# Performance work log

Measured on AMD Instinct MI355X. Metric: run time of the kernel, lower is better.

Reference implementation:

```python
import jax, jax.numpy as jnp
import numpy as np

N_NODES = 100000
N_EDGES = 1600000
D_NODE = 128
D_EDGE = 64
HID = 128
HEADS = 4
N_LAYERS = 3
LN_EPS = 1e-5
NEG_SLOPE = 0.2


def setup_inputs() -> dict:
    key = jax.random.key(0)
    ks = jax.random.split(key, 16)
    s = 0.05
    inp = {
        "node_features": jax.random.normal(ks[0], (N_NODES, D_NODE), jnp.float32),
        "edge_index": jax.random.randint(ks[1], (2, N_EDGES), 0, N_NODES, jnp.int32),
        "edge_attr": jax.random.normal(ks[2], (N_EDGES, D_EDGE), jnp.float32),
        # node encoder
        "W0": jax.random.normal(ks[3], (D_NODE, HID), jnp.float32) * s,
        "b0": jnp.zeros((HID,), jnp.float32),
        # per-layer stacked params [L, ...]
        "We": jax.random.normal(ks[4], (N_LAYERS, D_EDGE, HID), jnp.float32) * s,  # edge_encoder weight
        "be": jnp.zeros((N_LAYERS, HID), jnp.float32),
        "Wg": jax.random.normal(ks[5], (N_LAYERS, HID, HEADS * HID), jnp.float32) * s,  # GAT lin
        "att_src": jax.random.normal(ks[6], (N_LAYERS, HEADS, HID), jnp.float32) * s,
        "att_dst": jax.random.normal(ks[7], (N_LAYERS, HEADS, HID), jnp.float32) * s,
        "bg": jnp.zeros((N_LAYERS, HID), jnp.float32),  # GAT bias
        "gamma": jnp.ones((N_LAYERS, HID), jnp.float32),  # LayerNorm
        "beta": jnp.zeros((N_LAYERS, HID), jnp.float32),
    }
    return inp


def _layer_norm(x, g, b):
    mu = x.mean(-1, keepdims=True)
    var = ((x - mu) ** 2).mean(-1, keepdims=True)
    return (x - mu) * jax.lax.rsqrt(var + LN_EPS) * g + b


def _gat(x, src, dst, ew, Wg, att_s, att_d, bias, n):
    # x: [N,HID]; GATConv(heads=4, concat=False): average heads, +bias
    h = (x @ Wg).reshape(n, HEADS, HID)                     # [N,H,C]
    a_s = jnp.einsum("nhc,hc->nh", h, att_s)                # [N,H]
    a_d = jnp.einsum("nhc,hc->nh", h, att_d)
    logits = jax.nn.leaky_relu(a_s[src] + a_d[dst] + ew[:, None], NEG_SLOPE)  # [E,H]
    # segment softmax over incoming edges of each dst node
    m = jax.ops.segment_max(logits, dst, num_segments=n)    # self-loops => every node covered
    ex = jnp.exp(logits - m[dst])
    denom = jax.ops.segment_sum(ex, dst, num_segments=n)
    alpha = ex / denom[dst]                                 # [E,H]
    outs = []
    for hd in range(HEADS):  # loop over fixed small head count to cap peak memory
        msg = alpha[:, hd:hd + 1] * h[src, hd, :]           # [E,C]
        outs.append(jax.ops.segment_sum(msg, dst, num_segments=n))
    return jnp.stack(outs, 1).mean(1) + bias                # [N,HID]


def reference(node_features, edge_index, edge_attr, W0, b0, We, be, Wg, att_src, att_dst, bg, gamma, beta):
    n = node_features.shape[0]
    src, dst = edge_index[0], edge_index[1]
    # add self-loops (PyG GATConv default)
    loop = jnp.arange(n, dtype=src.dtype)
    src_f = jnp.concatenate([src, loop])
    dst_f = jnp.concatenate([dst, loop])

    x = jax.nn.relu(node_features @ W0 + b0)                # dropout = identity in eval
    for l in range(N_LAYERS):
        # edge_encoder(edge_attr).mean(-1) -> scalar edge weight added to attention logits
        ew = (edge_attr @ We[l] + be[l]).mean(-1)           # [E]
        ew_f = jnp.concatenate([ew, jnp.full((n,), ew.mean(), ew.dtype)])  # 'mean' fill for self-loops
        y = _gat(x, src_f, dst_f, ew_f, Wg[l], att_src[l], att_dst[l], bg[l], n)
        y = _layer_norm(y, gamma[l], beta[l])
        x = jax.nn.relu(x + y)
    return x
```

## Files before the change

### kernel.cpp

```cpp
#include <hip/hip_runtime.h>
#include <hip/hip_bf16.h>
#include <cstdio>

#define N_NODES 100000
#define N_EDGES 1600000
#define D_NODE 128
#define D_EDGE 64
#define HID 128
#define HEADS 4
#define N_LAYERS 3
#define LN_EPS 1e-5f
#define NEG_SLOPE 0.2f
#define EE (N_EDGES + N_NODES)
#define EW_GRID ((N_EDGES + 255) / 256)
#define SCAN_THREADS 1024
#define SCAN_CHUNK ((N_NODES + SCAN_THREADS - 1) / SCAN_THREADS)

typedef unsigned short bfraw;
using bf16x8 = __attribute__((ext_vector_type(8))) short;
using f32x4  = __attribute__((ext_vector_type(4))) float;

__device__ __forceinline__ float b2f(bfraw u) {
    return __uint_as_float(((unsigned)u) << 16);
}
__device__ __forceinline__ bfraw f2b(float f) {
    unsigned u = __float_as_uint(f);
    unsigned r = (u + 0x7fffu + ((u >> 16) & 1u)) >> 16;
    return (bfraw)r;
}
__device__ __forceinline__ float lrelu(float v) {
    return v > 0.f ? v : NEG_SLOPE * v;
}

__global__ __launch_bounds__(256) void prep_kernel(
    const float* __restrict__ We, const float* __restrict__ be,
    float* __restrict__ wem, float* __restrict__ bem) {
    int tid = threadIdx.x;
    if (tid < N_LAYERS * D_EDGE) {
        int l = tid / D_EDGE, d = tid % D_EDGE;
        const float* row = We + ((size_t)l * D_EDGE + d) * HID;
        float s = 0.f;
        for (int j = 0; j < HID; j++) s += row[j];
        wem[tid] = s * (1.0f / HID);
    } else if (tid < N_LAYERS * D_EDGE + N_LAYERS) {
        int l = tid - N_LAYERS * D_EDGE;
        const float* row = be + (size_t)l * HID;
        float s = 0.f;
        for (int j = 0; j < HID; j++) s += row[j];
        bem[l] = s * (1.0f / HID);
    }
}

__global__ __launch_bounds__(256) void ew_kernel(
    const float* __restrict__ ea, const float* __restrict__ wem,
    const float* __restrict__ bem, float* __restrict__ ew,
    float* __restrict__ partial) {
    __shared__ float wsh[N_LAYERS * D_EDGE];
    __shared__ float bsh[N_LAYERS];
    __shared__ float red[4][3];
    int tid = threadIdx.x;
    if (tid < N_LAYERS * D_EDGE) wsh[tid] = wem[tid];
    if (tid < N_LAYERS) bsh[tid] = bem[tid];
    __syncthreads();
    long long e = (long long)blockIdx.x * 256 + tid;
    float d0 = 0.f, d1 = 0.f, d2 = 0.f;
    if (e < N_EDGES) {
        const float4* row = (const float4*)(ea + (size_t)e * D_EDGE);
#pragma unroll
        for (int i = 0; i < D_EDGE / 4; i++) {
            float4 v = row[i];
            int c = i * 4;
            d0 += v.x * wsh[c] + v.y * wsh[c + 1] + v.z * wsh[c + 2] + v.w * wsh[c + 3];
            d1 += v.x * wsh[64 + c] + v.y * wsh[64 + c + 1] + v.z * wsh[64 + c + 2] + v.w * wsh[64 + c + 3];
            d2 += v.x * wsh[128 + c] + v.y * wsh[128 + c + 1] + v.z * wsh[128 + c + 2] + v.w * wsh[128 + c + 3];
        }
        ew[e] = d0 + bsh[0];
        ew[(size_t)N_EDGES + e] = d1 + bsh[1];
        ew[2 * (size_t)N_EDGES + e] = d2 + bsh[2];
    }
    float s0 = d0, s1 = d1, s2 = d2;
    for (int o = 32; o; o >>= 1) {
        s0 += __shfl_xor(s0, o);
        s1 += __shfl_xor(s1, o);
        s2 += __shfl_xor(s2, o);
    }
    int wid = tid >> 6;
    if ((tid & 63) == 0) {
        red[wid][0] = s0;
        red[wid][1] = s1;
        red[wid][2] = s2;
    }
    __syncthreads();
    if (tid < 3) {
        partial[(size_t)tid * EW_GRID + blockIdx.x] =
            red[0][tid] + red[1][tid] + red[2][tid] + red[3][tid];
    }
}

__global__ __launch_bounds__(256) void ewred_kernel(
    const float* __restrict__ partial, const float* __restrict__ bem,
    float* __restrict__ ewsum) {
    __shared__ float red[4];
    int l = blockIdx.x;
    int tid = threadIdx.x;
    float s = 0.f;
    for (int i = tid; i < EW_GRID; i += 256) s += partial[(size_t)l * EW_GRID + i];
    for (int o = 32; o; o >>= 1) s += __shfl_xor(s, o);
    int wid = tid >> 6;
    if ((tid & 63) == 0) red[wid] = s;
    __syncthreads();
    if (tid == 0)
        ewsum[l] = red[0] + red[1] + red[2] + red[3] + bem[l] * (float)N_EDGES;
}

__global__ __launch_bounds__(256) void deginit_kernel(int* __restrict__ deg) {
    int i = blockIdx.x * 256 + threadIdx.x;
    if (i < N_NODES) deg[i] = 1;
}

__global__ __launch_bounds__(256) void hist_kernel(
    const int* __restrict__ ei, int* __restrict__ deg) {
    int e = blockIdx.x * 256 + threadIdx.x;
    if (e < N_EDGES) atomicAdd(&deg[ei[N_EDGES + e]], 1);
}

__global__ __launch_bounds__(SCAN_THREADS) void scan_kernel(
    const int* __restrict__ deg, int* __restrict__ rowptr, int* __restrict__ woff) {
    __shared__ int part[SCAN_THREADS];
    int tid = threadIdx.x;
    int lo = tid * SCAN_CHUNK;
    int hi = lo + SCAN_CHUNK < N_NODES ? lo + SCAN_CHUNK : N_NODES;
    int s = 0;
    for (int i = lo; i < hi; i++) s += deg[i];
    part[tid] = s;
    __syncthreads();
    for (int off = 1; off < SCAN_THREADS; off <<= 1) {
        int t = (tid >= off) ? part[tid - off] : 0;
        __syncthreads();
        part[tid] += t;
        __syncthreads();
    }
    int run = (tid == 0) ? 0 : part[tid - 1];
    for (int i = lo; i < hi; i++) {
        rowptr[i] = run;
        woff[i] = run + 1;
        run += deg[i];
    }
    if (tid == 0) rowptr[N_NODES] = EE;
}

__global__ __launch_bounds__(256) void scatter_kernel(
    const int* __restrict__ ei, const float* __restrict__ ew,
    int* __restrict__ woff, int* __restrict__ csr_src,
    float* __restrict__ csr_ew) {
    int e = blockIdx.x * 256 + threadIdx.x;
    if (e >= N_EDGES) return;
    int d = ei[N_EDGES + e];
    int pos = atomicAdd(&woff[d], 1);
    csr_src[pos] = ei[e];
    csr_ew[pos] = ew[e];
    csr_ew[(size_t)EE + pos] = ew[(size_t)N_EDGES + e];
    csr_ew[2 * (size_t)EE + pos] = ew[2 * (size_t)N_EDGES + e];
}

__global__ __launch_bounds__(256) void selfloop_kernel(
    const int* __restrict__ rowptr, const float* __restrict__ ewsum,
    int* __restrict__ csr_src, float* __restrict__ csr_ew) {
    int d = blockIdx.x * 256 + threadIdx.x;
    if (d >= N_NODES) return;
    int pos = rowptr[d];
    csr_src[pos] = d;
    csr_ew[pos] = ewsum[0] * (1.0f / N_EDGES);
    csr_ew[(size_t)EE + pos] = ewsum[1] * (1.0f / N_EDGES);
    csr_ew[2 * (size_t)EE + pos] = ewsum[2] * (1.0f / N_EDGES);
}

__global__ __launch_bounds__(256) void castnf_kernel(
    const float* __restrict__ in, bfraw* __restrict__ out, int n4) {
    int i = blockIdx.x * 256 + threadIdx.x;
    if (i >= n4) return;
    float4 v = *(const float4*)(in + (size_t)i * 4);
    ushort4 u;
    u.x = f2b(v.x); u.y = f2b(v.y); u.z = f2b(v.z); u.w = f2b(v.w);
    *(ushort4*)(out + (size_t)i * 4) = u;
}

__global__ __launch_bounds__(256) void tcast_kernel(
    const float* __restrict__ in, bfraw* __restrict__ out, int lgN, int total) {
    int t = blockIdx.x * 256 + threadIdx.x;
    if (t >= total) return;
    int k = t & 127;
    int n = (t >> 7) & ((1 << lgN) - 1);
    int l = t >> (7 + lgN);
    out[t] = f2b(in[((size_t)l << (7 + lgN)) + ((size_t)k << lgN) + n]);
}

template <int EPI>
__global__ __launch_bounds__(256) void gemm_mfma_kernel(
    const bfraw* __restrict__ A, const bfraw* __restrict__ Bt,
    const float* __restrict__ bias, bfraw* __restrict__ outb,
    float* __restrict__ outf, int M, int N) {
    __shared__ short Alds[64 * 136];
    __shared__ short Blds[64 * 136];
    int tid = threadIdx.x;
    int m0 = blockIdx.y * 64;
    int n0 = blockIdx.x * 64;
    {
        int li = tid;
#pragma unroll
        for (int i = 0; i < 4; i++, li += 256) {
            int row = li >> 4, ch = li & 15;
            uint4 v = make_uint4(0u, 0u, 0u, 0u);
            if (m0 + row < M)
                v = *(const uint4*)(A + (size_t)(m0 + row) * 128 + ch * 8);
            *(uint4*)&Alds[row * 136 + ch * 8] = v;
            uint4 bv = *(const uint4*)(Bt + (size_t)(n0 + row) * 128 + ch * 8);
            *(uint4*)&Blds[row * 136 + ch * 8] = bv;
        }
    }
    __syncthreads();
    int w = tid >> 6, lane = tid & 63;
    int quad = lane >> 4, lr = lane & 15;
    bf16x8 bfr[4];
#pragma unroll
    for (int kc = 0; kc < 4; kc++)
        bfr[kc] = *(const bf16x8*)&Blds[(w * 16 + lr) * 136 + kc * 32 + quad * 8];
#pragma unroll
    for (int mt = 0; mt < 4; mt++) {
        f32x4 acc = {0.f, 0.f, 0.f, 0.f};
#pragma unroll
        for (int kc = 0; kc < 4; kc++) {
            bf16x8 afr = *(const bf16x8*)&Alds[(mt * 16 + lr) * 136 + kc * 32 + quad * 8];
            acc = __builtin_amdgcn_mfma_f32_16x16x32_bf16(afr, bfr[kc], acc, 0, 0, 0);
        }
        int col = n0 + w * 16 + lr;
#pragma unroll
        for (int r = 0; r < 4; r++) {
            int row = m0 + mt * 16 + quad * 4 + r;
            if (row >= M) continue;
            float v = acc[r];
            if (EPI == 1) {
                v += bias[col];
                v = fmaxf(v, 0.f);
                outf[(size_t)row * 128 + col] = v;
                outb[(size_t)row * 128 + col] = f2b(v);
            } else {
                outb[(size_t)row * N + col] = f2b(v);
            }
        }
    }
}

__global__ __launch_bounds__(256) void att_kernel(
    const bfraw* __restrict__ h, const float* __restrict__ att_s_l,
    const float* __restrict__ att_d_l, float* __restrict__ a_s, float* __restrict__ a_d) {
    __shared__ float ss[HEADS * HID], sd[HEADS * HID];
    int tid = threadIdx.x;
    for (int i = tid; i < HEADS * HID; i += 256) {
        ss[i] = att_s_l[i];
        sd[i] = att_d_l[i];
    }
    __syncthreads();
    long long gid = (long long)blockIdx.x * 256 + tid;
    if (gid >= (long long)N_NODES * HEADS) return;
    int n = (int)(gid >> 2), hd = (int)(gid & 3);
    const uint4* hv = (const uint4*)(h + (size_t)n * (HEADS * HID) + hd * HID);
    const float* ssp = ss + hd * HID;
    const float* sdp = sd + hd * HID;
    float s = 0.f, d = 0.f;
#pragma unroll
    for (int i = 0; i < 16; i++) {
        uint4 u = hv[i];
        unsigned wv[4] = {u.x, u.y, u.z, u.w};
#pragma unroll
        for (int j = 0; j < 4; j++) {
            float lo = __uint_as_float(wv[j] << 16);
            float hi = __uint_as_float(wv[j] & 0xffff0000u);
            int c = i * 8 + j * 2;
            s += lo * ssp[c] + hi * ssp[c + 1];
            d += lo * sdp[c] + hi * sdp[c + 1];
        }
    }
    a_s[gid] = s;
    a_d[gid] = d;
}

__device__ __forceinline__ void accum8(float* acc, uint4 u, float e) {
    unsigned wv[4] = {u.x, u.y, u.z, u.w};
#pragma unroll
    for (int j = 0; j < 4; j++) {
        acc[2 * j]     += e * __uint_as_float(wv[j] << 16);
        acc[2 * j + 1] += e * __uint_as_float(wv[j] & 0xffff0000u);
    }
}

__global__ __launch_bounds__(256) void agg_sm_ln_kernel(
    const int* __restrict__ rowptr, const int* __restrict__ csr_src,
    const float* __restrict__ ewl, const float* __restrict__ a_s,
    const float* __restrict__ a_d, const bfraw* __restrict__ h,
    const float* __restrict__ bg, const float* __restrict__ gamma,
    const float* __restrict__ beta, float* __restrict__ x, bfraw* __restrict__ xb) {
    int node = blockIdx.x * 4 + (threadIdx.x >> 6);
    int lane = threadIdx.x & 63;
    if (node >= N_NODES) return;
    int head = lane >> 4;
    int c8 = (lane & 15) * 8;
    int rs = rowptr[node], re = rowptr[node + 1];
    float ad = a_d[(size_t)node * HEADS + head];
    const bfraw* hb = h + head * HID + c8;

    float m = -1e30f, den = 0.f;
    float acc[8];
#pragma unroll
    for (int k = 0; k < 8; k++) acc[k] = 0.f;

    int i = rs;
    for (; i + 4 <= re; i += 4) {
        int s0 = csr_src[i],     s1 = csr_src[i + 1];
        int s2 = csr_src[i + 2], s3 = csr_src[i + 3];
        float w0 = ewl[i],     w1 = ewl[i + 1];
        float w2 = ewl[i + 2], w3 = ewl[i + 3];
        uint4 u0 = *(const uint4*)(hb + (size_t)s0 * (HEADS * HID));
        uint4 u1 = *(const uint4*)(hb + (size_t)s1 * (HEADS * HID));
        uint4 u2 = *(const uint4*)(hb + (size_t)s2 * (HEADS * HID));
        uint4 u3 = *(const uint4*)(hb + (size_t)s3 * (HEADS * HID));
        float as0 = a_s[(size_t)s0 * HEADS + head];
        float as1 = a_s[(size_t)s1 * HEADS + head];
        float as2 = a_s[(size_t)s2 * HEADS + head];
        float as3 = a_s[(size_t)s3 * HEADS + head];
        float l0 = lrelu(as0 + ad + w0);
        float l1 = lrelu(as1 + ad + w1);
        float l2 = lrelu(as2 + ad + w2);
        float l3 = lrelu(as3 + ad + w3);
        float mx = fmaxf(fmaxf(l0, l1), fmaxf(l2, l3));
        if (mx > m) {
            float c = __expf(m - mx);
            den *= c;
#pragma unroll
            for (int k = 0; k < 8; k++) acc[k] *= c;
            m = mx;
        }
        float e0 = __expf(l0 - m), e1 = __expf(l1 - m);
        float e2 = __expf(l2 - m), e3 = __expf(l3 - m);
        den += e0 + e1 + e2 + e3;
        accum8(acc, u0, e0);
        accum8(acc, u1, e1);
        accum8(acc, u2, e2);
        accum8(acc, u3, e3);
    }
    for (; i < re; i++) {
        int s = csr_src[i];
        float w = ewl[i];
        uint4 u = *(const uint4*)(hb + (size_t)s * (HEADS * HID));
        float as = a_s[(size_t)s * HEADS + head];
        float l0 = lrelu(as + ad + w);
        if (l0 > m) {
            float c = __expf(m - l0);
            den *= c;
#pragma unroll
            for (int k = 0; k < 8; k++) acc[k] *= c;
            m = l0;
        }
        float e = __expf(l0 - m);
        den += e;
        accum8(acc, u, e);
    }

    float iv = 1.f / den;
    float y[8];
    float sum = 0.f;
#pragma unroll
    for (int k = 0; k < 8; k++) {
        float v = acc[k] * iv;
        v += __shfl_xor(v, 16);
        v += __shfl_xor(v, 32);
        y[k] = 0.25f * v + bg[c8 + k];
        sum += y[k];
    }
#pragma unroll
    for (int o = 8; o; o >>= 1) sum += __shfl_xor(sum, o);
    float mu = sum * (1.f / HID);
    float vs = 0.f;
#pragma unroll
    for (int k = 0; k < 8; k++) {
        float d = y[k] - mu;
        vs += d * d;
    }
#pragma unroll
    for (int o = 8; o; o >>= 1) vs += __shfl_xor(vs, o);
    float r = rsqrtf(vs * (1.f / HID) + LN_EPS);

    if (lane < 16) {
        float4 xv0 = *(const float4*)(x + (size_t)node * HID + c8);
        float4 xv1 = *(const float4*)(x + (size_t)node * HID + c8 + 4);
        float xv[8] = {xv0.x, xv0.y, xv0.z, xv0.w, xv1.x, xv1.y, xv1.z, xv1.w};
        float o8[8];
#pragma unroll
        for (int k = 0; k < 8; k++) {
            float o = (y[k] - mu) * r * gamma[c8 + k] + beta[c8 + k];
            o8[k] = fmaxf(xv[k] + o, 0.f);
        }
        *(float4*)(x + (size_t)node * HID + c8) = make_float4(o8[0], o8[1], o8[2], o8[3]);
        *(float4*)(x + (size_t)node * HID + c8 + 4) = make_float4(o8[4], o8[5], o8[6], o8[7]);
        uint4 ub;
        ub.x = (unsigned)f2b(o8[0]) | ((unsigned)f2b(o8[1]) << 16);
        ub.y = (unsigned)f2b(o8[2]) | ((unsigned)f2b(o8[3]) << 16);
        ub.z = (unsigned)f2b(o8[4]) | ((unsigned)f2b(o8[5]) << 16);
        ub.w = (unsigned)f2b(o8[6]) | ((unsigned)f2b(o8[7]) << 16);
        *(uint4*)(xb + (size_t)node * HID + c8) = ub;
    }
}

extern "C" void kernel_launch(void* const* d_in, const int* in_sizes, int n_in,
                              void* d_out, int out_size, void* d_ws, size_t ws_size,
                              hipStream_t stream) {
    const float* nf      = (const float*)d_in[0];
    const int*   ei      = (const int*)d_in[1];
    const float* ea      = (const float*)d_in[2];
    const float* W0      = (const float*)d_in[3];
    const float* b0      = (const float*)d_in[4];
    const float* We      = (const float*)d_in[5];
    const float* be      = (const float*)d_in[6];
    const float* Wg      = (const float*)d_in[7];
    const float* att_src = (const float*)d_in[8];
    const float* att_dst = (const float*)d_in[9];
    const float* bg      = (const float*)d_in[10];
    const float* gamma   = (const float*)d_in[11];
    const float* beta    = (const float*)d_in[12];
    float* x = (float*)d_out;

    char* p = (char*)d_ws;
    auto alloc = [&](size_t bytes) -> void* {
        void* r = (void*)p;
        p += (bytes + 255) & ~(size_t)255;
        return r;
    };
    bfraw*  h       = (bfraw*)alloc((size_t)N_NODES * HEADS * HID * sizeof(bfraw));
    float4* alpha   = (float4*)alloc((size_t)EE * sizeof(float4));
    bfraw*  xb      = (bfraw*)alloc((size_t)N_NODES * HID * sizeof(bfraw));
    float*  a_s     = (float*)alloc((size_t)N_NODES * HEADS * sizeof(float));
    float*  a_d     = (float*)alloc((size_t)N_NODES * HEADS * sizeof(float));
    float*  ew      = (float*)alloc((size_t)N_LAYERS * N_EDGES * sizeof(float));
    int*    csr_src = (int*)alloc((size_t)EE * sizeof(int));
    float*  csr_ew  = (float*)alloc((size_t)N_LAYERS * EE * sizeof(float));
    int*    rowptr  = (int*)alloc((size_t)(N_NODES + 1) * sizeof(int));
    int*    deg     = (int*)alloc((size_t)N_NODES * sizeof(int));
    int*    woff    = (int*)alloc((size_t)N_NODES * sizeof(int));
    float*  wem     = (float*)alloc((size_t)N_LAYERS * D_EDGE * sizeof(float));
    float*  bem     = (float*)alloc((size_t)N_LAYERS * sizeof(float));
    float*  ewsum   = (float*)alloc((size_t)N_LAYERS * sizeof(float));
    float*  partial = (float*)alloc((size_t)N_LAYERS * EW_GRID * sizeof(float));
    bfraw*  W0bt    = (bfraw*)alloc((size_t)HID * D_NODE * sizeof(bfraw));
    bfraw*  Wgbt    = (bfraw*)alloc((size_t)N_LAYERS * HEADS * HID * HID * sizeof(bfraw));
    size_t need = (size_t)(p - (char*)d_ws);
    if (need > ws_size) {
        fprintf(stderr, "kernel_launch: workspace too small: need %zu have %zu\n", need, ws_size);
        return;
    }
    bfraw* nfb = (bfraw*)alpha;

    prep_kernel<<<1, 256, 0, stream>>>(We, be, wem, bem);
    ew_kernel<<<EW_GRID, 256, 0, stream>>>(ea, wem, bem, ew, partial);
    ewred_kernel<<<N_LAYERS, 256, 0, stream>>>(partial, bem, ewsum);

    deginit_kernel<<<(N_NODES + 255) / 256, 256, 0, stream>>>(deg);
    hist_kernel<<<(N_EDGES + 255) / 256, 256, 0, stream>>>(ei, deg);
    scan_kernel<<<1, SCAN_THREADS, 0, stream>>>(deg, rowptr, woff);
    scatter_kernel<<<(N_EDGES + 255) / 256, 256, 0, stream>>>(ei, ew, woff, csr_src, csr_ew);
    selfloop_kernel<<<(N_NODES + 255) / 256, 256, 0, stream>>>(rowptr, ewsum, csr_src, csr_ew);

    castnf_kernel<<<((N_NODES * D_NODE / 4) + 255) / 256, 256, 0, stream>>>(
        nf, nfb, N_NODES * D_NODE / 4);
    tcast_kernel<<<(HID * D_NODE + 255) / 256, 256, 0, stream>>>(
        W0, W0bt, 7, HID * D_NODE);
    tcast_kernel<<<(N_LAYERS * HID * HEADS * HID + 255) / 256, 256, 0, stream>>>(
        Wg, Wgbt, 9, N_LAYERS * HID * HEADS * HID);

    gemm_mfma_kernel<1><<<dim3(HID / 64, (N_NODES + 63) / 64), 256, 0, stream>>>(
        nfb, W0bt, b0, xb, x, N_NODES, HID);

    for (int l = 0; l < N_LAYERS; l++) {
        gemm_mfma_kernel<0><<<dim3(HEADS * HID / 64, (N_NODES + 63) / 64), 256, 0, stream>>>(
            xb, Wgbt + (size_t)l * HEADS * HID * HID, nullptr, h, nullptr,
            N_NODES, HEADS * HID);
        att_kernel<<<((long long)N_NODES * HEADS + 255) / 256, 256, 0, stream>>>(
            h, att_src + (size_t)l * HEADS * HID, att_dst + (size_t)l * HEADS * HID, a_s, a_d);
        agg_sm_ln_kernel<<<(N_NODES + 3) / 4, 256, 0, stream>>>(
            rowptr, csr_src, csr_ew + (size_t)l * EE, a_s, a_d, h,
            bg + (size_t)l * HID, gamma + (size_t)l * HID,
            beta + (size_t)l * HID, x, xb);
    }
}
```

Before: 2.126 ms.

## Pack CSR src and edge weights into uint4, fuse edge-weight with scatter

Fuses the edge-weight projection into the CSR scatter kernel, which now writes one packed uint4 record (src index plus three per-layer weights) per edge. This removes the intermediate ew buffer and the separate scatter pass. The aggregation kernel is templated on layer to select its weight field, unrolled to 8 edges per iteration, and uses a lazy max rescale threshold of 8 to skip most rescaling. The trade-offs are that each layer reads 16 bytes per edge instead of 8, and the lazy rescale lets exponent arguments grow up to about 8.

```diff
diff --git a/kernel.cpp b/kernel.cpp
--- a/kernel.cpp
+++ b/kernel.cpp
@@ -51,68 +51,6 @@
     }
 }
 
-__global__ __launch_bounds__(256) void ew_kernel(
-    const float* __restrict__ ea, const float* __restrict__ wem,
-    const float* __restrict__ bem, float* __restrict__ ew,
-    float* __restrict__ partial) {
-    __shared__ float wsh[N_LAYERS * D_EDGE];
-    __shared__ float bsh[N_LAYERS];
-    __shared__ float red[4][3];
-    int tid = threadIdx.x;
-    if (tid < N_LAYERS * D_EDGE) wsh[tid] = wem[tid];
-    if (tid < N_LAYERS) bsh[tid] = bem[tid];
-    __syncthreads();
-    long long e = (long long)blockIdx.x * 256 + tid;
-    float d0 = 0.f, d1 = 0.f, d2 = 0.f;
-    if (e < N_EDGES) {
-        const float4* row = (const float4*)(ea + (size_t)e * D_EDGE);
-#pragma unroll
-        for (int i = 0; i < D_EDGE / 4; i++) {
-            float4 v = row[i];
-            int c = i * 4;
-            d0 += v.x * wsh[c] + v.y * wsh[c + 1] + v.z * wsh[c + 2] + v.w * wsh[c + 3];
-            d1 += v.x * wsh[64 + c] + v.y * wsh[64 + c + 1] + v.z * wsh[64 + c + 2] + v.w * wsh[64 + c + 3];
-            d2 += v.x * wsh[128 + c] + v.y * wsh[128 + c + 1] + v.z * wsh[128 + c + 2] + v.w * wsh[128 + c + 3];
-        }
-        ew[e] = d0 + bsh[0];
-        ew[(size_t)N_EDGES + e] = d1 + bsh[1];
-        ew[2 * (size_t)N_EDGES + e] = d2 + bsh[2];
-    }
-    float s0 = d0, s1 = d1, s2 = d2;
-    for (int o = 32; o; o >>= 1) {
-        s0 += __shfl_xor(s0, o);
-        s1 += __shfl_xor(s1, o);
-        s2 += __shfl_xor(s2, o);
-    }
-    int wid = tid >> 6;
-    if ((tid & 63) == 0) {
-        red[wid][0] = s0;
-        red[wid][1] = s1;
-        red[wid][2] = s2;
-    }
-    __syncthreads();
-    if (tid < 3) {
-        partial[(size_t)tid * EW_GRID + blockIdx.x] =
-            red[0][tid] + red[1][tid] + red[2][tid] + red[3][tid];
-    }
-}
-
-__global__ __launch_bounds__(256) void ewred_kernel(
-    const float* __restrict__ partial, const float* __restrict__ bem,
-    float* __restrict__ ewsum) {
-    __shared__ float red[4];
-    int l = blockIdx.x;
-    int tid = threadIdx.x;
-    float s = 0.f;
-    for (int i = tid; i < EW_GRID; i += 256) s += partial[(size_t)l * EW_GRID + i];
-    for (int o = 32; o; o >>= 1) s += __shfl_xor(s, o);
-    int wid = tid >> 6;
-    if ((tid & 63) == 0) red[wid] = s;
-    __syncthreads();
-    if (tid == 0)
-        ewsum[l] = red[0] + red[1] + red[2] + red[3] + bem[l] * (float)N_EDGES;
-}
-
 __global__ __launch_bounds__(256) void deginit_kernel(int* __restrict__ deg) {
     int i = blockIdx.x * 256 + threadIdx.x;
     if (i < N_NODES) deg[i] = 1;
@@ -149,30 +87,87 @@
     if (tid == 0) rowptr[N_NODES] = EE;
 }
 
-__global__ __launch_bounds__(256) void scatter_kernel(
-    const int* __restrict__ ei, const float* __restrict__ ew,
-    int* __restrict__ woff, int* __restrict__ csr_src,
-    float* __restrict__ csr_ew) {
-    int e = blockIdx.x * 256 + threadIdx.x;
-    if (e >= N_EDGES) return;
-    int d = ei[N_EDGES + e];
-    int pos = atomicAdd(&woff[d], 1);
-    csr_src[pos] = ei[e];
-    csr_ew[pos] = ew[e];
-    csr_ew[(size_t)EE + pos] = ew[(size_t)N_EDGES + e];
-    csr_ew[2 * (size_t)EE + pos] = ew[2 * (size_t)N_EDGES + e];
+__global__ __launch_bounds__(256) void ewscat_kernel(
+    const float* __restrict__ ea, const int* __restrict__ ei,
+    const float* __restrict__ wem, const float* __restrict__ bem,
+    int* __restrict__ woff, uint4* __restrict__ csrq,
+    float* __restrict__ partial) {
+    __shared__ float wsh[N_LAYERS * D_EDGE];
+    __shared__ float bsh[N_LAYERS];
+    __shared__ float red[4][3];
+    int tid = threadIdx.x;
+    if (tid < N_LAYERS * D_EDGE) wsh[tid] = wem[tid];
+    if (tid < N_LAYERS) bsh[tid] = bem[tid];
+    __syncthreads();
+    long long e = (long long)blockIdx.x * 256 + tid;
+    float d0 = 0.f, d1 = 0.f, d2 = 0.f;
+    if (e < N_EDGES) {
+        const float4* row = (const float4*)(ea + (size_t)e * D_EDGE);
+#pragma unroll
+        for (int i = 0; i < D_EDGE / 4; i++) {
+            float4 v = row[i];
+            int c = i * 4;
+            d0 += v.x * wsh[c] + v.y * wsh[c + 1] + v.z * wsh[c + 2] + v.w * wsh[c + 3];
+            d1 += v.x * wsh[64 + c] + v.y * wsh[64 + c + 1] + v.z * wsh[64 + c + 2] + v.w * wsh[64 + c + 3];
+            d2 += v.x * wsh[128 + c] + v.y * wsh[128 + c + 1] + v.z * wsh[128 + c + 2] + v.w * wsh[128 + c + 3];
+        }
+        int src = ei[e];
+        int dst = ei[N_EDGES + e];
+        int pos = atomicAdd(&woff[dst], 1);
+        uint4 q;
+        q.x = (unsigned)src;
+        q.y = __float_as_uint(d0 + bsh[0]);
+        q.z = __float_as_uint(d1 + bsh[1]);
+        q.w = __float_as_uint(d2 + bsh[2]);
+        csrq[pos] = q;
+    }
+    float s0 = d0, s1 = d1, s2 = d2;
+    for (int o = 32; o; o >>= 1) {
+        s0 += __shfl_xor(s0, o);
+        s1 += __shfl_xor(s1, o);
+        s2 += __shfl_xor(s2, o);
+    }
+    int wid = tid >> 6;
+    if ((tid & 63) == 0) {
+        red[wid][0] = s0;
+        red[wid][1] = s1;
+        red[wid][2] = s2;
+    }
+    __syncthreads();
+    if (tid < 3) {
+        partial[(size_t)tid * EW_GRID + blockIdx.x] =
+            red[0][tid] + red[1][tid] + red[2][tid] + red[3][tid];
+    }
+}
+
+__global__ __launch_bounds__(256) void ewred_kernel(
+    const float* __restrict__ partial, const float* __restrict__ bem,
+    float* __restrict__ ewsum) {
+    __shared__ float red[4];
+    int l = blockIdx.x;
+    int tid = threadIdx.x;
+    float s = 0.f;
+    for (int i = tid; i < EW_GRID; i += 256) s += partial[(size_t)l * EW_GRID + i];
+    for (int o = 32; o; o >>= 1) s += __shfl_xor(s, o);
+    int wid = tid >> 6;
+    if ((tid & 63) == 0) red[wid] = s;
+    __syncthreads();
+    if (tid == 0)
+        ewsum[l] = red[0] + red[1] + red[2] + red[3] + bem[l] * (float)N_EDGES;
 }
 
 __global__ __launch_bounds__(256) void selfloop_kernel(
     const int* __restrict__ rowptr, const float* __restrict__ ewsum,
-    int* __restrict__ csr_src, float* __restrict__ csr_ew) {
+    uint4* __restrict__ csrq) {
     int d = blockIdx.x * 256 + threadIdx.x;
     if (d >= N_NODES) return;
     int pos = rowptr[d];
-    csr_src[pos] = d;
-    csr_ew[pos] = ewsum[0] * (1.0f / N_EDGES);
-    csr_ew[(size_t)EE + pos] = ewsum[1] * (1.0f / N_EDGES);
-    csr_ew[2 * (size_t)EE + pos] = ewsum[2] * (1.0f / N_EDGES);
+    uint4 q;
+    q.x = (unsigned)d;
+    q.y = __float_as_uint(ewsum[0] * (1.0f / N_EDGES));
+    q.z = __float_as_uint(ewsum[1] * (1.0f / N_EDGES));
+    q.w = __float_as_uint(ewsum[2] * (1.0f / N_EDGES));
+    csrq[pos] = q;
 }
 
 __global__ __launch_bounds__(256) void castnf_kernel(
@@ -294,12 +289,13 @@
     }
 }
 
+template <int L>
 __global__ __launch_bounds__(256) void agg_sm_ln_kernel(
-    const int* __restrict__ rowptr, const int* __restrict__ csr_src,
-    const float* __restrict__ ewl, const float* __restrict__ a_s,
-    const float* __restrict__ a_d, const bfraw* __restrict__ h,
-    const float* __restrict__ bg, const float* __restrict__ gamma,
-    const float* __restrict__ beta, float* __restrict__ x, bfraw* __restrict__ xb) {
+    const int* __restrict__ rowptr, const uint4* __restrict__ csrq,
+    const float* __restrict__ a_s, const float* __restrict__ a_d,
+    const bfraw* __restrict__ h, const float* __restrict__ bg,
+    const float* __restrict__ gamma, const float* __restrict__ beta,
+    float* __restrict__ x, bfraw* __restrict__ xb) {
     int node = blockIdx.x * 4 + (threadIdx.x >> 6);
     int lane = threadIdx.x & 63;
     if (node >= N_NODES) return;
@@ -315,46 +311,88 @@
     for (int k = 0; k < 8; k++) acc[k] = 0.f;
 
     int i = rs;
-    for (; i + 4 <= re; i += 4) {
-        int s0 = csr_src[i],     s1 = csr_src[i + 1];
-        int s2 = csr_src[i + 2], s3 = csr_src[i + 3];
-        float w0 = ewl[i],     w1 = ewl[i + 1];
-        float w2 = ewl[i + 2], w3 = ewl[i + 3];
-        uint4 u0 = *(const uint4*)(hb + (size_t)s0 * (HEADS * HID));
-        uint4 u1 = *(const uint4*)(hb + (size_t)s1 * (HEADS * HID));
-        uint4 u2 = *(const uint4*)(hb + (size_t)s2 * (HEADS * HID));
-        uint4 u3 = *(const uint4*)(hb + (size_t)s3 * (HEADS * HID));
-        float as0 = a_s[(size_t)s0 * HEADS + head];
-        float as1 = a_s[(size_t)s1 * HEADS + head];
-        float as2 = a_s[(size_t)s2 * HEADS + head];
-        float as3 = a_s[(size_t)s3 * HEADS + head];
-        float l0 = lrelu(as0 + ad + w0);
-        float l1 = lrelu(as1 + ad + w1);
-        float l2 = lrelu(as2 + ad + w2);
-        float l3 = lrelu(as3 + ad + w3);
-        float mx = fmaxf(fmaxf(l0, l1), fmaxf(l2, l3));
-        if (mx > m) {
+    for (; i + 8 <= re; i += 8) {
+        uint4 q[8];
+#pragma unroll
+        for (int k = 0; k < 8; k++) q[k] = csrq[i + k];
+        uint4 u[8];
+        float as[8];
+#pragma unroll
+        for (int k = 0; k < 8; k++) {
+            int s = (int)q[k].x;
+            u[k] = *(const uint4*)(hb + (size_t)s * (HEADS * HID));
+            as[k] = a_s[(size_t)s * HEADS + head];
+        }
+        float lg[8];
+#pragma unroll
+        for (int k = 0; k < 8; k++) {
+            float w = (L == 0) ? __uint_as_float(q[k].y)
+                    : (L == 1) ? __uint_as_float(q[k].z)
+                               : __uint_as_float(q[k].w);
+            lg[k] = lrelu(as[k] + ad + w);
+        }
+        float mx = lg[0];
+#pragma unroll
+        for (int k = 1; k < 8; k++) mx = fmaxf(mx, lg[k]);
+        if (mx > m + 8.f) {
             float c = __expf(m - mx);
             den *= c;
 #pragma unroll
             for (int k = 0; k < 8; k++) acc[k] *= c;
             m = mx;
         }
-        float e0 = __expf(l0 - m), e1 = __expf(l1 - m);
-        float e2 = __expf(l2 - m), e3 = __expf(l3 - m);
-        den += e0 + e1 + e2 + e3;
-        accum8(acc, u0, e0);
-        accum8(acc, u1, e1);
-        accum8(acc, u2, e2);
-        accum8(acc, u3, e3);
+#pragma unroll
+        for (int k = 0; k < 8; k++) {
+            float e = __expf(lg[k] - m);
+            den += e;
+            accum8(acc, u[k], e);
+        }
+    }
+    for (; i + 4 <= re; i += 4) {
+        uint4 q[4];
+#pragma unroll
+        for (int k = 0; k < 4; k++) q[k] = csrq[i + k];
+        uint4 u[4];
+        float as[4];
+#pragma unroll
+        for (int k = 0; k < 4; k++) {
+            int s = (int)q[k].x;
+            u[k] = *(const uint4*)(hb + (size_t)s * (HEADS * HID));
+            as[k] = a_s[(size_t)s * HEADS + head];
+        }
+        float lg[4];
+#pragma unroll
+        for (int k = 0; k < 4; k++) {
+            float w = (L == 0) ? __uint_as_float(q[k].y)
+                    : (L == 1) ? __uint_as_float(q[k].z)
+                               : __uint_as_float(q[k].w);
+            lg[k] = lrelu(as[k] + ad + w);
+        }
+        float mx = fmaxf(fmaxf(lg[0], lg[1]), fmaxf(lg[2], lg[3]));
+        if (mx > m + 8.f) {
+            float c = __expf(m - mx);
+            den *= c;
+#pragma unroll
+            for (int k = 0; k < 8; k++) acc[k] *= c;
+            m = mx;
+        }
+#pragma unroll
+        for (int k = 0; k < 4; k++) {
+            float e = __expf(lg[k] - m);
+            den += e;
+            accum8(acc, u[k], e);
+        }
     }
     for (; i < re; i++) {
-        int s = csr_src[i];
-        float w = ewl[i];
+        uint4 q = csrq[i];
+        int s = (int)q.x;
+        float w = (L == 0) ? __uint_as_float(q.y)
+                : (L == 1) ? __uint_as_float(q.z)
+                           : __uint_as_float(q.w);
         uint4 u = *(const uint4*)(hb + (size_t)s * (HEADS * HID));
         float as = a_s[(size_t)s * HEADS + head];
         float l0 = lrelu(as + ad + w);
-        if (l0 > m) {
+        if (l0 > m + 8.f) {
             float c = __expf(m - l0);
             den *= c;
 #pragma unroll
@@ -436,13 +474,11 @@
         return r;
     };
     bfraw*  h       = (bfraw*)alloc((size_t)N_NODES * HEADS * HID * sizeof(bfraw));
-    float4* alpha   = (float4*)alloc((size_t)EE * sizeof(float4));
+    bfraw*  nfb     = (bfraw*)alloc((size_t)N_NODES * D_NODE * sizeof(bfraw));
     bfraw*  xb      = (bfraw*)alloc((size_t)N_NODES * HID * sizeof(bfraw));
     float*  a_s     = (float*)alloc((size_t)N_NODES * HEADS * sizeof(float));
     float*  a_d     = (float*)alloc((size_t)N_NODES * HEADS * sizeof(float));
-    float*  ew      = (float*)alloc((size_t)N_LAYERS * N_EDGES * sizeof(float));
-    int*    csr_src = (int*)alloc((size_t)EE * sizeof(int));
-    float*  csr_ew  = (float*)alloc((size_t)N_LAYERS * EE * sizeof(float));
+    uint4*  csrq    = (uint4*)alloc((size_t)EE * sizeof(uint4));
     int*    rowptr  = (int*)alloc((size_t)(N_NODES + 1) * sizeof(int));
     int*    deg     = (int*)alloc((size_t)N_NODES * sizeof(int));
     int*    woff    = (int*)alloc((size_t)N_NODES * sizeof(int));
@@ -457,17 +493,15 @@
         fprintf(stderr, "kernel_launch: workspace too small: need %zu have %zu\n", need, ws_size);
         return;
     }
-    bfraw* nfb = (bfraw*)alpha;
 
     prep_kernel<<<1, 256, 0, stream>>>(We, be, wem, bem);
-    ew_kernel<<<EW_GRID, 256, 0, stream>>>(ea, wem, bem, ew, partial);
-    ewred_kernel<<<N_LAYERS, 256, 0, stream>>>(partial, bem, ewsum);
 
     deginit_kernel<<<(N_NODES + 255) / 256, 256, 0, stream>>>(deg);
     hist_kernel<<<(N_EDGES + 255) / 256, 256, 0, stream>>>(ei, deg);
     scan_kernel<<<1, SCAN_THREADS, 0, stream>>>(deg, rowptr, woff);
-    scatter_kernel<<<(N_EDGES + 255) / 256, 256, 0, stream>>>(ei, ew, woff, csr_src, csr_ew);
-    selfloop_kernel<<<(N_NODES + 255) / 256, 256, 0, stream>>>(rowptr, ewsum, csr_src, csr_ew);
+    ewscat_kernel<<<EW_GRID, 256, 0, stream>>>(ea, ei, wem, bem, woff, csrq, partial);
+    ewred_kernel<<<N_LAYERS, 256, 0, stream>>>(partial, bem, ewsum);
+    selfloop_kernel<<<(N_NODES + 255) / 256, 256, 0, stream>>>(rowptr, ewsum, csrq);
 
     castnf_kernel<<<((N_NODES * D_NODE / 4) + 255) / 256, 256, 0, stream>>>(
         nf, nfb, N_NODES * D_NODE / 4);
@@ -485,9 +519,17 @@
             N_NODES, HEADS * HID);
         att_kernel<<<((long long)N_NODES * HEADS + 255) / 256, 256, 0, stream>>>(
             h, att_src + (size_t)l * HEADS * HID, att_dst + (size_t)l * HEADS * HID, a_s, a_d);
-        agg_sm_ln_kernel<<<(N_NODES + 3) / 4, 256, 0, stream>>>(
-            rowptr, csr_src, csr_ew + (size_t)l * EE, a_s, a_d, h,
-            bg + (size_t)l * HID, gamma + (size_t)l * HID,
-            beta + (size_t)l * HID, x, xb);
-    }
-}
+        if (l == 0)
+            agg_sm_ln_kernel<0><<<(N_NODES + 3) / 4, 256, 0, stream>>>(
+                rowptr, csrq, a_s, a_d, h, bg + (size_t)l * HID,
+                gamma + (size_t)l * HID, beta + (size_t)l * HID, x, xb);
+        else if (l == 1)
+            agg_sm_ln_kernel<1><<<(N_NODES + 3) / 4, 256, 0, stream>>>(
+                rowptr, csrq, a_s, a_d, h, bg + (size_t)l * HID,
+                gamma + (size_t)l * HID, beta + (size_t)l * HID, x, xb);
+        else
+            agg_sm_ln_kernel<2><<<(N_NODES + 3) / 4, 256, 0, stream>>>(
+                rowptr, csrq, a_s, a_d, h, bg + (size_t)l * HID,
+                gamma + (size_t)l * HID, beta + (size_t)l * HID, x, xb);
+    }
+}
```

Result: faster. 2.018 ms (-5.1%).
